# Kernel tuning notes

Hardware: AMD Instinct MI355X
Metric: run time of the kernel (lower is better)

## Reference

```python
import jax, jax.numpy as jnp
import numpy as np

B, DEC_T, ENC_T = 64, 128, 1024
H, ENC_D, ATTN, VOCAB = 512, 512, 512, 128


def setup_inputs() -> dict:
    key = jax.random.key(0)
    ks = jax.random.split(key, 12)
    s = 0.05
    return {
        "inputs": jax.random.randint(ks[0], (B, DEC_T), 0, 127),
        "encoder_outputs": jax.random.normal(ks[1], (B, ENC_T, ENC_D), jnp.float32),
        "embedding": jax.random.normal(ks[2], (VOCAB, H), jnp.float32) * s,
        "w_ih": jax.random.normal(ks[3], (3 * H, H + ENC_D), jnp.float32) * s,
        "w_hh": jax.random.normal(ks[4], (3 * H, H), jnp.float32) * s,
        "b_ih": jnp.zeros((3 * H,), jnp.float32),
        "b_hh": jnp.zeros((3 * H,), jnp.float32),
        "attn_wq": jax.random.normal(ks[5], (ATTN, H), jnp.float32) * s,
        "attn_wv": jax.random.normal(ks[6], (ATTN, ENC_D), jnp.float32) * s,
        "attn_conv_w": jax.random.normal(ks[7], (ATTN, 1, 3), jnp.float32) * s,
        "attn_conv_b": jnp.zeros((ATTN,), jnp.float32),
        "attn_bias": jnp.zeros((ATTN,), jnp.float32),
        "attn_v": jax.random.normal(ks[8], (ATTN,), jnp.float32) * s,
        "fc_w": jax.random.normal(ks[9], (VOCAB, H + ENC_D), jnp.float32) * s,
        "fc_b": jnp.zeros((VOCAB,), jnp.float32),
    }


def reference(inputs, encoder_outputs, embedding, w_ih, w_hh, b_ih, b_hh,
              attn_wq, attn_wv, attn_conv_w, attn_conv_b, attn_bias, attn_v,
              fc_w, fc_b):
    emb = embedding[inputs]  # (B, dec_T, H); no eos in inputs so filter is identity
    # precompute encoder value projection once (reused every step)
    enc_proj = jnp.einsum('bte,ae->bta', encoder_outputs, attn_wv)  # (B, enc_T, A)

    def gru_step(h, x):
        gi = x @ w_ih.T + b_ih  # (B, 3H)
        gh = h @ w_hh.T + b_hh
        r = jax.nn.sigmoid(gi[:, :H] + gh[:, :H])
        z = jax.nn.sigmoid(gi[:, H:2 * H] + gh[:, H:2 * H])
        n = jnp.tanh(gi[:, 2 * H:] + r * gh[:, 2 * H:])
        return (1.0 - z) * n + z * h

    def step(carry, x_t):
        h, context, attn_w = carry
        rnn_in = jnp.concatenate([x_t, context], axis=1)  # (B, H+enc_D)
        h = gru_step(h, rnn_in)  # output == new hidden for 1-layer GRU
        # location-aware attention: conv over previous attention weights
        conv = jax.lax.conv_general_dilated(
            attn_w[:, None, :], attn_conv_w, (1,), ((1, 1),),
            dimension_numbers=('NCH', 'OIH', 'NCH'))  # (B, A, enc_T)
        conv_feat = conv.transpose(0, 2, 1) + attn_conv_b  # (B, enc_T, A)
        q = h @ attn_wq.T  # (B, A)
        e = jnp.tanh(q[:, None, :] + enc_proj + conv_feat + attn_bias)
        score = jnp.einsum('bta,a->bt', e, attn_v)  # (B, enc_T)
        attn_w = jax.nn.softmax(score, axis=-1)
        context = jnp.einsum('bt,bte->be', attn_w, encoder_outputs)  # (B, enc_D)
        out_cat = jnp.concatenate([h, context], axis=1)  # (B, H+enc_D)
        pred = jax.nn.log_softmax(out_cat @ fc_w.T + fc_b, axis=-1)  # (B, V)
        return (h, context, attn_w), (pred, attn_w, out_cat)

    init = (jnp.zeros((B, H), emb.dtype),
            jnp.zeros((B, ENC_D), emb.dtype),
            jnp.zeros((B, ENC_T), emb.dtype))
    _, (y, aw, oc) = jax.lax.scan(step, init, emb.transpose(1, 0, 2))
    # back to batch-major: (B, dec_T, *)
    return (y.transpose(1, 0, 2), aw.transpose(1, 0, 2), oc.transpose(1, 0, 2))
```

## Files before the change

kernel.cpp:

```cpp
#include <hip/hip_runtime.h>
#include <stdint.h>

#define BB 64
#define SS 128
#define EE 1024
#define HH 512
#define DD 512
#define AA 512
#define VV 128
#define KX 1536
#define NC 2048
#define NSC 8
#define NCP 4

#define AW_OFF ((size_t)BB*SS*VV)
#define OC_OFF (AW_OFF + (size_t)BB*SS*EE)

typedef unsigned short u16;

__device__ __forceinline__ float sigmoid_f(float x){
  return __builtin_amdgcn_rcpf(1.f + __expf(-x));
}
__device__ __forceinline__ float tanh_f(float x){
  float e = __expf(2.f*x);
  return 1.f - 2.f*__builtin_amdgcn_rcpf(e + 1.f);
}
__device__ __forceinline__ u16 f2bf(float f){
  uint32_t u = __float_as_uint(f);
  return (u16)((u + 0x7fffu + ((u>>16)&1u)) >> 16);
}

__global__ void k_build(const float* __restrict__ w_ih, const float* __restrict__ w_hh,
                        const float* __restrict__ b_ih, const float* __restrict__ b_hh,
                        const float* __restrict__ wq,   const float* __restrict__ wv,
                        const float* __restrict__ fc_w,
                        float* __restrict__ Wbig, float* __restrict__ wqT,
                        float* __restrict__ wvT,  float* __restrict__ fcT,
                        float* __restrict__ bias_big){
  int i = blockIdx.x*256 + threadIdx.x;
  const int NW = KX*NC;
  if (i < NW){
    int k = i >> 11, c = i & (NC-1);
    float v;
    if (c < 1024)      v = (k < 1024) ? w_ih[c*1024 + k] : w_hh[c*512 + (k-1024)];
    else if (c < 1536) v = (k < 1024) ? w_ih[c*1024 + k] : 0.f;
    else               v = (k >= 1024) ? w_hh[(c-512)*512 + (k-1024)] : 0.f;
    Wbig[i] = v; return;
  }
  i -= NW;
  if (i < 512*512){ int j = i >> 9, a = i & 511; wqT[i] = wq[a*512 + j]; return; }
  i -= 512*512;
  if (i < 512*512){ int e = i >> 9, a = i & 511; wvT[i] = wv[a*512 + e]; return; }
  i -= 512*512;
  if (i < 1024*128){ int k = i >> 7, v = i & 127; fcT[i] = fc_w[v*1024 + k]; return; }
  i -= 1024*128;
  if (i < NC){
    float bv;
    if (i < 1024)      bv = b_ih[i] + b_hh[i];
    else if (i < 1536) bv = b_ih[i];
    else               bv = b_hh[i - 512];
    bias_big[i] = bv;
  }
}

__global__ __launch_bounds__(256) void k_encp(const float* __restrict__ enc,
                                              const float* __restrict__ wvT,
                                              const float* __restrict__ abias,
                                              const float* __restrict__ convb,
                                              u16* __restrict__ encp){
  __shared__ float As[64][36];
  __shared__ float Bs[32][68];
  int tid = threadIdx.x;
  int r0 = blockIdx.x * 64;
  int a0 = blockIdx.y * 64;
  float4 acc[4];
  #pragma unroll
  for (int r = 0; r < 4; ++r) acc[r] = make_float4(0.f,0.f,0.f,0.f);
  int rl = tid >> 2, kl0 = (tid & 3) * 8;
  int kl2 = tid >> 3, al0 = (tid & 7) * 8;
  int br = (tid >> 4) * 4, cc = (tid & 15) * 4;
  for (int kk = 0; kk < 512; kk += 32){
    float4 av0 = *(const float4*)&enc[(size_t)(r0+rl)*512 + kk + kl0];
    float4 av1 = *(const float4*)&enc[(size_t)(r0+rl)*512 + kk + kl0 + 4];
    float4 bv0 = *(const float4*)&wvT[(size_t)(kk+kl2)*512 + a0 + al0];
    float4 bv1 = *(const float4*)&wvT[(size_t)(kk+kl2)*512 + a0 + al0 + 4];
    __syncthreads();
    *(float4*)&As[rl][kl0]     = av0;
    *(float4*)&As[rl][kl0+4]   = av1;
    *(float4*)&Bs[kl2][al0]    = bv0;
    *(float4*)&Bs[kl2][al0+4]  = bv1;
    __syncthreads();
    #pragma unroll
    for (int i = 0; i < 32; ++i){
      float4 b4 = *(const float4*)&Bs[i][cc];
      float x0 = As[br][i], x1 = As[br+1][i], x2 = As[br+2][i], x3 = As[br+3][i];
      acc[0].x += x0*b4.x; acc[0].y += x0*b4.y; acc[0].z += x0*b4.z; acc[0].w += x0*b4.w;
      acc[1].x += x1*b4.x; acc[1].y += x1*b4.y; acc[1].z += x1*b4.z; acc[1].w += x1*b4.w;
      acc[2].x += x2*b4.x; acc[2].y += x2*b4.y; acc[2].z += x2*b4.z; acc[2].w += x2*b4.w;
      acc[3].x += x3*b4.x; acc[3].y += x3*b4.y; acc[3].z += x3*b4.z; acc[3].w += x3*b4.w;
    }
  }
  int a = a0 + cc;
  float b0f = abias[a]   + convb[a];
  float b1f = abias[a+1] + convb[a+1];
  float b2f_ = abias[a+2] + convb[a+2];
  float b3f = abias[a+3] + convb[a+3];
  #pragma unroll
  for (int r = 0; r < 4; ++r){
    size_t row = (size_t)(r0 + br + r);
    ushort4 pk;
    pk.x = f2bf(acc[r].x + b0f);
    pk.y = f2bf(acc[r].y + b1f);
    pk.z = f2bf(acc[r].z + b2f_);
    pk.w = f2bf(acc[r].w + b3f);
    *(ushort4*)&encp[row*512 + a] = pk;
  }
}

__global__ __launch_bounds__(256) void k_encbf(const float* __restrict__ enc,
                                               u16* __restrict__ enc_bf){
  size_t i = ((size_t)blockIdx.x*256 + threadIdx.x) * 4;
  float4 v = *(const float4*)&enc[i];
  ushort4 pk;
  pk.x = f2bf(v.x); pk.y = f2bf(v.y); pk.z = f2bf(v.z); pk.w = f2bf(v.w);
  *(ushort4*)&enc_bf[i] = pk;
}

__global__ __launch_bounds__(256) void k_ggemm_fc(const int* __restrict__ inputs,
                                                  const float* __restrict__ emb,
                                                  const float* __restrict__ ctxp,
                                                  const float* __restrict__ sump,
                                                  const float* __restrict__ h,
                                                  const float* __restrict__ Wbig,
                                                  float* __restrict__ Gp,
                                                  const float* __restrict__ fcT,
                                                  const float* __restrict__ fc_b,
                                                  float* __restrict__ rs_buf,
                                                  float* __restrict__ out,
                                                  int s, int gemm_nb, int sfc){
  int tid = threadIdx.x;
  if ((int)blockIdx.x < gemm_nb){
    __shared__ float Xs[64][36];
    __shared__ float Ws[32][68];
    __shared__ float rs_l[64];
    int bid = blockIdx.x;
    int c0 = (bid & 31) * 64;
    int kc = bid >> 5;
    int kbase = kc * 192;
    bool t0 = (s == 0);
    if (!t0 && tid < 64){
      float ssum = 0.f;
      #pragma unroll
      for (int p2 = 0; p2 < NSC; ++p2) ssum += sump[p2*64 + tid];
      rs_l[tid] = __builtin_amdgcn_rcpf(ssum);
    }
    float4 acc[4];
    #pragma unroll
    for (int r = 0; r < 4; ++r) acc[r] = make_float4(0.f,0.f,0.f,0.f);
    int bl = tid >> 2, kl0 = (tid & 3) * 8;
    int kw = tid >> 3, cl0 = (tid & 7) * 8;
    int br = (tid >> 4) * 4, cc = (tid & 15) * 4;
    const float* emb_b = emb + (size_t)inputs[bl*SS + s]*HH;
    __syncthreads();
    for (int kk = 0; kk < 192; kk += 32){
      float xv[8];
      #pragma unroll
      for (int u = 0; u < 8; ++u){
        int kg = kbase + kk + kl0 + u;
        float v;
        if (kg < 512)       v = emb_b[kg];
        else if (kg < 1024){
          if (t0) v = 0.f;
          else {
            int d = kg - 512;
            float t = 0.f;
            #pragma unroll
            for (int p2 = 0; p2 < NCP; ++p2) t += ctxp[(size_t)(p2*64+bl)*512 + d];
            v = t * rs_l[bl];
          }
        }
        else                v = t0 ? 0.f : h[bl*512 + kg - 1024];
        xv[u] = v;
      }
      float4 w1 = *(const float4*)&Wbig[(size_t)(kbase+kk+kw)*NC + c0 + cl0];
      float4 w2 = *(const float4*)&Wbig[(size_t)(kbase+kk+kw)*NC + c0 + cl0 + 4];
      __syncthreads();
      *(float4*)&Xs[bl][kl0]   = make_float4(xv[0],xv[1],xv[2],xv[3]);
      *(float4*)&Xs[bl][kl0+4] = make_float4(xv[4],xv[5],xv[6],xv[7]);
      *(float4*)&Ws[kw][cl0]   = w1;
      *(float4*)&Ws[kw][cl0+4] = w2;
      __syncthreads();
      #pragma unroll
      for (int i = 0; i < 32; ++i){
        float4 b4 = *(const float4*)&Ws[i][cc];
        float x0 = Xs[br][i], x1 = Xs[br+1][i], x2 = Xs[br+2][i], x3 = Xs[br+3][i];
        acc[0].x += x0*b4.x; acc[0].y += x0*b4.y; acc[0].z += x0*b4.z; acc[0].w += x0*b4.w;
        acc[1].x += x1*b4.x; acc[1].y += x1*b4.y; acc[1].z += x1*b4.z; acc[1].w += x1*b4.w;
        acc[2].x += x2*b4.x; acc[2].y += x2*b4.y; acc[2].z += x2*b4.z; acc[2].w += x2*b4.w;
        acc[3].x += x3*b4.x; acc[3].y += x3*b4.y; acc[3].z += x3*b4.z; acc[3].w += x3*b4.w;
      }
    }
    #pragma unroll
    for (int r = 0; r < 4; ++r)
      *(float4*)&Gp[(size_t)(kc*64 + br + r)*NC + c0 + cc] = acc[r];
  } else {
    if (sfc < 0) return;
    __shared__ float oc_l[1024];
    __shared__ float lp[2][128];
    __shared__ float l_l[128];
    int b = blockIdx.x - gemm_nb;
    float ssum = 0.f;
    #pragma unroll
    for (int p2 = 0; p2 < NSC; ++p2) ssum += sump[p2*64 + b];
    float rs = __builtin_amdgcn_rcpf(ssum);
    if (tid == 0) rs_buf[b] = rs;
    oc_l[tid]       = h[b*512 + tid];
    oc_l[tid + 256] = h[b*512 + tid + 256];
    int d0 = tid*2;
    float a0 = 0.f, a1 = 0.f;
    #pragma unroll
    for (int cc2 = 0; cc2 < NCP; ++cc2){
      float2 p2v = *(const float2*)&ctxp[(size_t)(cc2*64 + b)*512 + d0];
      a0 += p2v.x; a1 += p2v.y;
    }
    a0 *= rs; a1 *= rs;
    oc_l[512 + d0]     = a0;
    oc_l[512 + d0 + 1] = a1;
    size_t oco = OC_OFF + (size_t)(b*SS + sfc)*1024 + 512 + d0;
    out[oco]     = a0;
    out[oco + 1] = a1;
    __syncthreads();
    int v = tid & 127, half = tid >> 7;
    float acc = 0.f;
    #pragma unroll 8
    for (int k = 0; k < 512; ++k)
      acc += oc_l[half*512 + k] * fcT[(size_t)(half*512 + k)*128 + v];
    lp[half][v] = acc;
    __syncthreads();
    if (tid < 128) l_l[tid] = lp[0][tid] + lp[1][tid] + fc_b[tid];
    __syncthreads();
    if (tid < 128){
      float m = -1e30f;
      for (int i = 0; i < 128; ++i) m = fmaxf(m, l_l[i]);
      float sm = 0.f;
      for (int i = 0; i < 128; ++i) sm += __expf(l_l[i] - m);
      out[(size_t)(b*SS + sfc)*VV + tid] = l_l[tid] - m - __logf(sm);
    }
  }
}

__global__ __launch_bounds__(256) void k_gate_q(const float* __restrict__ Gp,
                                                const float* __restrict__ bias_big,
                                                float* __restrict__ h,
                                                const float* __restrict__ wqT,
                                                float* __restrict__ qp,
                                                float* __restrict__ out, int s){
  __shared__ float h_l[512];
  int tid = threadIdx.x;
  int jt = blockIdx.x, bt = blockIdx.y;
  bool t0 = (s == 0);
  #pragma unroll
  for (int it = 0; it < 2; ++it){
    int item = tid + it*256;
    int bi = item >> 6, jl = item & 63;
    int b = bt*8 + bi, j = jt*64 + jl;
    float s0=0.f, s1=0.f, s2=0.f, s3=0.f;
    #pragma unroll
    for (int kc = 0; kc < 8; ++kc){
      const float* g = Gp + (size_t)(kc*64 + b)*NC;
      s0 += g[j]; s1 += g[512+j]; s2 += g[1024+j]; s3 += g[1536+j];
    }
    float r = sigmoid_f(s0 + bias_big[j]);
    float z = sigmoid_f(s1 + bias_big[512+j]);
    float n = tanh_f(s2 + bias_big[1024+j] + r*(s3 + bias_big[1536+j]));
    float hold = t0 ? 0.f : h[b*512 + j];
    float hn = (1.f - z)*n + z*hold;
    h_l[item] = hn;
    h[b*512 + j] = hn;
    out[OC_OFF + (size_t)(b*SS + s)*1024 + j] = hn;
  }
  __syncthreads();
  int a0 = tid*2;
  float2 acc8[8];
  #pragma unroll
  for (int bi = 0; bi < 8; ++bi) acc8[bi] = make_float2(0.f, 0.f);
  for (int j = 0; j < 64; ++j){
    float2 w = *(const float2*)&wqT[(size_t)(jt*64 + j)*512 + a0];
    #pragma unroll
    for (int bi = 0; bi < 8; ++bi){
      float hv = h_l[bi*64 + j];
      acc8[bi].x += hv*w.x; acc8[bi].y += hv*w.y;
    }
  }
  #pragma unroll
  for (int bi = 0; bi < 8; ++bi)
    *(float2*)&qp[(size_t)(jt*64 + bt*8 + bi)*512 + a0] = acc8[bi];
}

__global__ __launch_bounds__(1024, 8) void k_score(const float* __restrict__ qp,
                                                   const float* __restrict__ attn_v,
                                                   const float* __restrict__ conv_w,
                                                   const u16* __restrict__ encp,
                                                   const float* __restrict__ expsc_prev,
                                                   float* __restrict__ expsc_cur,
                                                   const float* __restrict__ rs_buf,
                                                   float* __restrict__ sump,
                                                   float* __restrict__ out, int s){
  __shared__ float q_l[512], v_l[512], c0_l[512], c1_l[512], c2_l[512];
  __shared__ float ew_l[128];
  int tid = threadIdx.x;
  int et = blockIdx.x, b = blockIdx.y;
  if (tid < 512){
    float qq = 0.f;
    #pragma unroll
    for (int jt = 0; jt < 8; ++jt) qq += qp[(size_t)(jt*64 + b)*512 + tid];
    q_l[tid]  = qq;
    v_l[tid]  = attn_v[tid];
    c0_l[tid] = conv_w[tid*3 + 0];
    c1_l[tid] = conv_w[tid*3 + 1];
    c2_l[tid] = conv_w[tid*3 + 2];
  }
  __syncthreads();
  int wave = tid >> 6, lane = tid & 63;
  float q8[8], v8[8], c08[8], c18[8], c28[8];
  #pragma unroll
  for (int i = 0; i < 8; ++i){
    int a = lane*8 + i;
    q8[i] = q_l[a]; v8[i] = v_l[a]; c08[i] = c0_l[a]; c18[i] = c1_l[a]; c28[i] = c2_l[a];
  }
  float rs_prev = (s > 0) ? rs_buf[b] : 0.f;
  const float* prev = expsc_prev + (size_t)b*EE;
  #pragma unroll
  for (int eu = 0; eu < 8; ++eu){
    int e_loc = wave*8 + eu;
    int e = et*128 + e_loc;
    float wl = 0.f, wc = 0.f, wr = 0.f;
    if (s > 0){
      wc = prev[e] * rs_prev;
      wl = (e > 0)    ? prev[e-1]*rs_prev : 0.f;
      wr = (e < EE-1) ? prev[e+1]*rs_prev : 0.f;
    }
    uint4 pk = *(const uint4*)(encp + ((size_t)(b*EE + e)*512 + lane*8));
    uint32_t ua[4] = {pk.x, pk.y, pk.z, pk.w};
    float acc = 0.f;
    #pragma unroll
    for (int p = 0; p < 4; ++p){
      float plo = __uint_as_float(ua[p] << 16);
      float phi = __uint_as_float(ua[p] & 0xffff0000u);
      int ii = p*2;
      float v0 = q8[ii]   + plo + c08[ii]*wl   + c18[ii]*wc   + c28[ii]*wr;
      acc += tanh_f(v0) * v8[ii];
      float v1 = q8[ii+1] + phi + c08[ii+1]*wl + c18[ii+1]*wc + c28[ii+1]*wr;
      acc += tanh_f(v1) * v8[ii+1];
    }
    #pragma unroll
    for (int off = 32; off; off >>= 1) acc += __shfl_xor(acc, off, 64);
    if (lane == 0) ew_l[e_loc] = __expf(acc);
  }
  __syncthreads();
  if (tid < 128){
    int e = et*128 + tid;
    expsc_cur[(size_t)b*EE + e] = ew_l[tid];
    if (s > 0) out[AW_OFF + (size_t)(b*SS + (s-1))*EE + e] = prev[e]*rs_prev;
  }
  if (tid < 64){
    float t2 = ew_l[tid] + ew_l[tid + 64];
    #pragma unroll
    for (int off = 32; off; off >>= 1) t2 += __shfl_xor(t2, off, 64);
    if (tid == 0) sump[et*64 + b] = t2;
  }
}

__global__ __launch_bounds__(512, 8) void k_ctx(const u16* __restrict__ enc_bf,
                                                const float* __restrict__ expsc_cur,
                                                float* __restrict__ ctxp){
  __shared__ float w_l[256];
  __shared__ float redc[8][512];
  int tid = threadIdx.x;
  int c = blockIdx.x, b = blockIdx.y;
  if (tid < 256) w_l[tid] = expsc_cur[(size_t)b*EE + c*256 + tid];
  __syncthreads();
  int es = tid >> 6, lane = tid & 63;
  int d0 = lane * 8;
  float acc8[8];
  #pragma unroll
  for (int i = 0; i < 8; ++i) acc8[i] = 0.f;
  #pragma unroll 4
  for (int i = 0; i < 32; ++i){
    int e_loc = es*32 + i;
    uint4 pk = *(const uint4*)(enc_bf + ((size_t)(b*EE + c*256 + e_loc)*512 + d0));
    float w = w_l[e_loc];
    uint32_t ua[4] = {pk.x, pk.y, pk.z, pk.w};
    #pragma unroll
    for (int p = 0; p < 4; ++p){
      acc8[p*2]   += w * __uint_as_float(ua[p] << 16);
      acc8[p*2+1] += w * __uint_as_float(ua[p] & 0xffff0000u);
    }
  }
  #pragma unroll
  for (int i = 0; i < 8; ++i) redc[es][d0 + i] = acc8[i];
  __syncthreads();
  if (tid < 128){
    int d = tid * 4;
    float4 t = make_float4(0.f,0.f,0.f,0.f);
    #pragma unroll
    for (int e2 = 0; e2 < 8; ++e2){
      float4 r4 = *(const float4*)&redc[e2][d];
      t.x += r4.x; t.y += r4.y; t.z += r4.z; t.w += r4.w;
    }
    *(float4*)&ctxp[(size_t)(c*64 + b)*512 + d] = t;
  }
}

__global__ __launch_bounds__(256) void k_tail(const float* __restrict__ h,
                                              const float* __restrict__ ctxp,
                                              const float* __restrict__ sump,
                                              const float* __restrict__ expsc,
                                              const float* __restrict__ fcT,
                                              const float* __restrict__ fc_b,
                                              float* __restrict__ out){
  __shared__ float oc_l[1024];
  __shared__ float lp[2][128];
  __shared__ float l_l[128];
  int tid = threadIdx.x, b = blockIdx.x;
  const int sfc = SS - 1;
  float ssum = 0.f;
  #pragma unroll
  for (int p2 = 0; p2 < NSC; ++p2) ssum += sump[p2*64 + b];
  float rs = __builtin_amdgcn_rcpf(ssum);
  #pragma unroll
  for (int i = 0; i < 4; ++i){
    int e = i*256 + tid;
    out[AW_OFF + (size_t)(b*SS + sfc)*EE + e] = expsc[(size_t)b*EE + e] * rs;
  }
  oc_l[tid]       = h[b*512 + tid];
  oc_l[tid + 256] = h[b*512 + tid + 256];
  int d0 = tid*2;
  float a0 = 0.f, a1 = 0.f;
  #pragma unroll
  for (int cc2 = 0; cc2 < NCP; ++cc2){
    float2 p2v = *(const float2*)&ctxp[(size_t)(cc2*64 + b)*512 + d0];
    a0 += p2v.x; a1 += p2v.y;
  }
  a0 *= rs; a1 *= rs;
  oc_l[512 + d0]     = a0;
  oc_l[512 + d0 + 1] = a1;
  size_t oco = OC_OFF + (size_t)(b*SS + sfc)*1024 + 512 + d0;
  out[oco]     = a0;
  out[oco + 1] = a1;
  __syncthreads();
  int v = tid & 127, half = tid >> 7;
  float acc = 0.f;
  #pragma unroll 8
  for (int k = 0; k < 512; ++k)
    acc += oc_l[half*512 + k] * fcT[(size_t)(half*512 + k)*128 + v];
  lp[half][v] = acc;
  __syncthreads();
  if (tid < 128) l_l[tid] = lp[0][tid] + lp[1][tid] + fc_b[tid];
  __syncthreads();
  if (tid < 128){
    float m = -1e30f;
    for (int i = 0; i < 128; ++i) m = fmaxf(m, l_l[i]);
    float sm = 0.f;
    for (int i = 0; i < 128; ++i) sm += __expf(l_l[i] - m);
    out[(size_t)(b*SS + sfc)*VV + tid] = l_l[tid] - m - __logf(sm);
  }
}

extern "C" void kernel_launch(void* const* d_in, const int* in_sizes, int n_in,
                              void* d_out, int out_size, void* d_ws, size_t ws_size,
                              hipStream_t stream){
  (void)in_sizes; (void)n_in; (void)out_size; (void)ws_size;
  const int*   inputs = (const int*)d_in[0];
  const float* enc    = (const float*)d_in[1];
  const float* emb    = (const float*)d_in[2];
  const float* w_ih   = (const float*)d_in[3];
  const float* w_hh   = (const float*)d_in[4];
  const float* b_ih   = (const float*)d_in[5];
  const float* b_hh   = (const float*)d_in[6];
  const float* wq     = (const float*)d_in[7];
  const float* wv     = (const float*)d_in[8];
  const float* convw  = (const float*)d_in[9];
  const float* convb  = (const float*)d_in[10];
  const float* abias  = (const float*)d_in[11];
  const float* av     = (const float*)d_in[12];
  const float* fcw    = (const float*)d_in[13];
  const float* fcb    = (const float*)d_in[14];
  float* out = (float*)d_out;

  char* p = (char*)d_ws;
  auto alloc = [&](size_t bytes)->char*{
    char* r = p; p += (bytes + 255) & ~(size_t)255; return r;
  };
  u16*   encp   = (u16*)  alloc((size_t)BB*EE*AA*2);
  u16*   enc_bf = (u16*)  alloc((size_t)BB*EE*DD*2);
  float* Wbig   = (float*)alloc((size_t)KX*NC*4);
  float* wqT    = (float*)alloc((size_t)512*512*4);
  float* wvT    = (float*)alloc((size_t)512*512*4);
  float* fcT    = (float*)alloc((size_t)1024*128*4);
  float* biasb  = (float*)alloc((size_t)NC*4);
  float* hbuf   = (float*)alloc((size_t)BB*HH*4);
  float* Gp     = (float*)alloc((size_t)8*BB*NC*4);
  float* qp     = (float*)alloc((size_t)8*BB*AA*4);
  float* exps0  = (float*)alloc((size_t)BB*EE*4);
  float* exps1  = (float*)alloc((size_t)BB*EE*4);
  float* sump   = (float*)alloc((size_t)NSC*BB*4);
  float* ctxp   = (float*)alloc((size_t)NCP*BB*DD*4);
  float* rs_buf = (float*)alloc((size_t)BB*4);

  int total0 = KX*NC + 512*512 + 512*512 + 1024*128 + NC;
  k_build<<<(total0 + 255)/256, 256, 0, stream>>>(w_ih, w_hh, b_ih, b_hh, wq, wv, fcw,
                                                  Wbig, wqT, wvT, fcT, biasb);
  k_encp<<<dim3(1024, 8), 256, 0, stream>>>(enc, wvT, abias, convb, encp);
  k_encbf<<<(BB*EE*DD/4 + 255)/256, 256, 0, stream>>>(enc, enc_bf);

  for (int s = 0; s < SS; ++s){
    int sfc = s - 1;
    int grid = (sfc >= 0) ? 320 : 256;
    float* e_prev = (s & 1) ? exps0 : exps1;
    float* e_cur  = (s & 1) ? exps1 : exps0;
    k_ggemm_fc<<<grid, 256, 0, stream>>>(inputs, emb, ctxp, sump, hbuf, Wbig, Gp,
                                         fcT, fcb, rs_buf, out, s, 256, sfc);
    k_gate_q<<<dim3(8, 8), 256, 0, stream>>>(Gp, biasb, hbuf, wqT, qp, out, s);
    k_score<<<dim3(8, 64), 1024, 0, stream>>>(qp, av, convw, encp,
                                              e_prev, e_cur, rs_buf, sump, out, s);
    k_ctx<<<dim3(4, 64), 512, 0, stream>>>(enc_bf, e_cur, ctxp);
  }
  k_tail<<<64, 256, 0, stream>>>(hbuf, ctxp, sump, exps1, fcT, fcb, out);
}
```

Measured before the change: 10.62 ms.

## Replace per-step kernel launches with persistent kernel using grid barriers

```diff
diff --git a/kernel.cpp b/kernel.cpp
--- a/kernel.cpp
+++ b/kernel.cpp
@@ -10,8 +10,10 @@
 #define VV 128
 #define KX 1536
 #define NC 2048
-#define NSC 8
+#define NKC 6
+#define NSC 4
 #define NCP 4
+#define NBLK 256
 
 #define AW_OFF ((size_t)BB*SS*VV)
 #define OC_OFF (AW_OFF + (size_t)BB*SS*EE)
@@ -126,344 +128,357 @@
   *(ushort4*)&enc_bf[i] = pk;
 }
 
-__global__ __launch_bounds__(256) void k_ggemm_fc(const int* __restrict__ inputs,
-                                                  const float* __restrict__ emb,
-                                                  const float* __restrict__ ctxp,
-                                                  const float* __restrict__ sump,
-                                                  const float* __restrict__ h,
-                                                  const float* __restrict__ Wbig,
-                                                  float* __restrict__ Gp,
-                                                  const float* __restrict__ fcT,
-                                                  const float* __restrict__ fc_b,
-                                                  float* __restrict__ rs_buf,
-                                                  float* __restrict__ out,
-                                                  int s, int gemm_nb, int sfc){
-  int tid = threadIdx.x;
-  if ((int)blockIdx.x < gemm_nb){
-    __shared__ float Xs[64][36];
-    __shared__ float Ws[32][68];
-    __shared__ float rs_l[64];
-    int bid = blockIdx.x;
-    int c0 = (bid & 31) * 64;
-    int kc = bid >> 5;
-    int kbase = kc * 192;
-    bool t0 = (s == 0);
-    if (!t0 && tid < 64){
+__device__ __forceinline__ void gbar(unsigned* bar, int bid){
+  __syncthreads();
+  if (threadIdx.x == 0){
+    unsigned* cnt1 = bar + (bid >> 4) * 32;
+    unsigned* cnt2 = bar + 512;
+    unsigned* gen  = bar + 544;
+    unsigned g = __hip_atomic_load(gen, __ATOMIC_RELAXED, __HIP_MEMORY_SCOPE_AGENT);
+    unsigned o1 = __hip_atomic_fetch_add(cnt1, 1u, __ATOMIC_ACQ_REL, __HIP_MEMORY_SCOPE_AGENT);
+    if (o1 == 15u){
+      __hip_atomic_store(cnt1, 0u, __ATOMIC_RELAXED, __HIP_MEMORY_SCOPE_AGENT);
+      unsigned o2 = __hip_atomic_fetch_add(cnt2, 1u, __ATOMIC_ACQ_REL, __HIP_MEMORY_SCOPE_AGENT);
+      if (o2 == 15u){
+        __hip_atomic_store(cnt2, 0u, __ATOMIC_RELAXED, __HIP_MEMORY_SCOPE_AGENT);
+        __hip_atomic_store(gen, g + 1u, __ATOMIC_RELEASE, __HIP_MEMORY_SCOPE_AGENT);
+      } else {
+        while (__hip_atomic_load(gen, __ATOMIC_ACQUIRE, __HIP_MEMORY_SCOPE_AGENT) == g)
+          __builtin_amdgcn_s_sleep(2);
+      }
+    } else {
+      while (__hip_atomic_load(gen, __ATOMIC_ACQUIRE, __HIP_MEMORY_SCOPE_AGENT) == g)
+        __builtin_amdgcn_s_sleep(2);
+    }
+  }
+  __syncthreads();
+}
+
+struct SmA { float Xs[64][36]; float Ws[32][68]; float rs_l[64]; };
+struct SmF { float oc[1024]; float lp[2][128]; float ll[128]; };
+struct SmB { float h_l[512]; };
+struct SmC { float q[512]; float v[512]; float c0[512]; float c1[512];
+             float c2[512]; float pw[260]; float ew[256]; float redc[8][512]; };
+union Smem { SmA a; SmF f; SmB b; SmC c; };
+
+__device__ __forceinline__ float score8(uint4 pk, float wl, float wc, float wr,
+                                        const float* q8, const float* v8,
+                                        const float* c08, const float* c18,
+                                        const float* c28){
+  uint32_t ua[4] = {pk.x, pk.y, pk.z, pk.w};
+  float acc = 0.f;
+  #pragma unroll
+  for (int p = 0; p < 4; ++p){
+    float plo = __uint_as_float(ua[p] << 16);
+    float phi = __uint_as_float(ua[p] & 0xffff0000u);
+    int ii = p*2;
+    float x0 = q8[ii]   + plo + c08[ii]*wl   + c18[ii]*wc   + c28[ii]*wr;
+    acc += tanh_f(x0) * v8[ii];
+    float x1 = q8[ii+1] + phi + c08[ii+1]*wl + c18[ii+1]*wc + c28[ii+1]*wr;
+    acc += tanh_f(x1) * v8[ii+1];
+  }
+  return acc;
+}
+
+__global__ __launch_bounds__(512, 2) void k_persist(
+    const int* __restrict__ inputs, const float* __restrict__ emb,
+    const float* __restrict__ Wbig, const float* __restrict__ biasb,
+    const float* __restrict__ wqT,  const float* __restrict__ fcT,
+    const float* __restrict__ fcb,  const float* __restrict__ av,
+    const float* __restrict__ convw,
+    const u16* __restrict__ encp,   const u16* __restrict__ enc_bf,
+    float* __restrict__ Gp, float* __restrict__ qp, float* __restrict__ hbuf,
+    float* __restrict__ exps0, float* __restrict__ exps1,
+    float* __restrict__ sump, float* __restrict__ ctxp,
+    float* __restrict__ rs_buf, unsigned* bar, float* __restrict__ out)
+{
+  __shared__ Smem sm;
+  const int tid = threadIdx.x, bid = blockIdx.x;
+
+  for (int s = 0; s < SS; ++s){
+    const bool t0 = (s == 0);
+    const float* eprev = (s & 1) ? exps0 : exps1;
+    float*       ecur  = (s & 1) ? exps1 : exps0;
+
+    if (bid < 192){
+      const int c0 = (bid & 31) * 64;
+      const int kc = bid >> 5;
+      const int kbase = kc * 256;
+      if (!t0 && tid < 64){
+        float ssum = 0.f;
+        #pragma unroll
+        for (int p2 = 0; p2 < NSC; ++p2) ssum += sump[p2*64 + tid];
+        sm.a.rs_l[tid] = __builtin_amdgcn_rcpf(ssum);
+      }
+      const int bl = tid >> 3, kl0 = (tid & 7) * 4;
+      const int kw = tid >> 4, cl0 = (tid & 15) * 4;
+      const int br = (tid >> 4) * 2, cc = (tid & 15) * 4;
+      const float* emb_b = emb + (size_t)inputs[bl*SS + s]*HH;
+      float4 acc0 = make_float4(0.f,0.f,0.f,0.f);
+      float4 acc1 = make_float4(0.f,0.f,0.f,0.f);
+      __syncthreads();
+      for (int kk = 0; kk < 256; kk += 32){
+        float xv[4];
+        #pragma unroll
+        for (int u = 0; u < 4; ++u){
+          int kg = kbase + kk + kl0 + u;
+          float v;
+          if (kg < 512)       v = emb_b[kg];
+          else if (kg < 1024){
+            if (t0) v = 0.f;
+            else {
+              int d = kg - 512;
+              float t = 0.f;
+              #pragma unroll
+              for (int p2 = 0; p2 < NCP; ++p2) t += ctxp[(size_t)(p2*64+bl)*512 + d];
+              v = t * sm.a.rs_l[bl];
+            }
+          }
+          else                v = t0 ? 0.f : hbuf[bl*512 + kg - 1024];
+          xv[u] = v;
+        }
+        float4 w1 = *(const float4*)&Wbig[(size_t)(kbase+kk+kw)*NC + c0 + cl0];
+        __syncthreads();
+        *(float4*)&sm.a.Xs[bl][kl0] = make_float4(xv[0],xv[1],xv[2],xv[3]);
+        *(float4*)&sm.a.Ws[kw][cl0] = w1;
+        __syncthreads();
+        #pragma unroll
+        for (int i = 0; i < 32; ++i){
+          float4 b4 = *(const float4*)&sm.a.Ws[i][cc];
+          float x0 = sm.a.Xs[br][i], x1 = sm.a.Xs[br+1][i];
+          acc0.x += x0*b4.x; acc0.y += x0*b4.y; acc0.z += x0*b4.z; acc0.w += x0*b4.w;
+          acc1.x += x1*b4.x; acc1.y += x1*b4.y; acc1.z += x1*b4.z; acc1.w += x1*b4.w;
+        }
+      }
+      *(float4*)&Gp[(size_t)(kc*64 + br    )*NC + c0 + cc] = acc0;
+      *(float4*)&Gp[(size_t)(kc*64 + br + 1)*NC + c0 + cc] = acc1;
+    } else if (!t0){
+      const int b = bid - 192;
       float ssum = 0.f;
       #pragma unroll
-      for (int p2 = 0; p2 < NSC; ++p2) ssum += sump[p2*64 + tid];
-      rs_l[tid] = __builtin_amdgcn_rcpf(ssum);
-    }
-    float4 acc[4];
-    #pragma unroll
-    for (int r = 0; r < 4; ++r) acc[r] = make_float4(0.f,0.f,0.f,0.f);
-    int bl = tid >> 2, kl0 = (tid & 3) * 8;
-    int kw = tid >> 3, cl0 = (tid & 7) * 8;
-    int br = (tid >> 4) * 4, cc = (tid & 15) * 4;
-    const float* emb_b = emb + (size_t)inputs[bl*SS + s]*HH;
-    __syncthreads();
-    for (int kk = 0; kk < 192; kk += 32){
-      float xv[8];
-      #pragma unroll
-      for (int u = 0; u < 8; ++u){
-        int kg = kbase + kk + kl0 + u;
-        float v;
-        if (kg < 512)       v = emb_b[kg];
-        else if (kg < 1024){
-          if (t0) v = 0.f;
-          else {
-            int d = kg - 512;
-            float t = 0.f;
-            #pragma unroll
-            for (int p2 = 0; p2 < NCP; ++p2) t += ctxp[(size_t)(p2*64+bl)*512 + d];
-            v = t * rs_l[bl];
-          }
-        }
-        else                v = t0 ? 0.f : h[bl*512 + kg - 1024];
-        xv[u] = v;
-      }
-      float4 w1 = *(const float4*)&Wbig[(size_t)(kbase+kk+kw)*NC + c0 + cl0];
-      float4 w2 = *(const float4*)&Wbig[(size_t)(kbase+kk+kw)*NC + c0 + cl0 + 4];
-      __syncthreads();
-      *(float4*)&Xs[bl][kl0]   = make_float4(xv[0],xv[1],xv[2],xv[3]);
-      *(float4*)&Xs[bl][kl0+4] = make_float4(xv[4],xv[5],xv[6],xv[7]);
-      *(float4*)&Ws[kw][cl0]   = w1;
-      *(float4*)&Ws[kw][cl0+4] = w2;
-      __syncthreads();
-      #pragma unroll
+      for (int p2 = 0; p2 < NSC; ++p2) ssum += sump[p2*64 + b];
+      const float rs = __builtin_amdgcn_rcpf(ssum);
+      if (tid == 0) rs_buf[b] = rs;
+      if (tid < 256){
+        sm.f.oc[tid]     = hbuf[b*512 + tid];
+        sm.f.oc[tid+256] = hbuf[b*512 + tid + 256];
+        int d0 = tid*2;
+        float a0 = 0.f, a1 = 0.f;
+        #pragma unroll
+        for (int cc2 = 0; cc2 < NCP; ++cc2){
+          float2 pv = *(const float2*)&ctxp[(size_t)(cc2*64 + b)*512 + d0];
+          a0 += pv.x; a1 += pv.y;
+        }
+        a0 *= rs; a1 *= rs;
+        sm.f.oc[512+d0]   = a0;
+        sm.f.oc[512+d0+1] = a1;
+        size_t oco = OC_OFF + (size_t)(b*SS + (s-1))*1024 + 512 + d0;
+        out[oco]     = a0;
+        out[oco + 1] = a1;
+      }
+      __syncthreads();
+      if (tid < 256){
+        int v = tid & 127, half = tid >> 7;
+        float acc = 0.f;
+        #pragma unroll 8
+        for (int k = 0; k < 512; ++k)
+          acc += sm.f.oc[half*512 + k] * fcT[(size_t)(half*512 + k)*128 + v];
+        sm.f.lp[half][v] = acc;
+      }
+      __syncthreads();
+      if (tid < 128) sm.f.ll[tid] = sm.f.lp[0][tid] + sm.f.lp[1][tid] + fcb[tid];
+      __syncthreads();
+      if (tid < 128){
+        float m = -1e30f;
+        for (int i = 0; i < 128; ++i) m = fmaxf(m, sm.f.ll[i]);
+        float smm = 0.f;
+        for (int i = 0; i < 128; ++i) smm += __expf(sm.f.ll[i] - m);
+        out[(size_t)(b*SS + (s-1))*VV + tid] = sm.f.ll[tid] - m - __logf(smm);
+      }
+    }
+    gbar(bar, bid);
+
+    if (bid < 64){
+      const int jt = bid & 7, bt = bid >> 3;
+      const int bi = tid >> 6, jl = tid & 63;
+      const int b = bt*8 + bi, j = jt*64 + jl;
+      float s0=0.f, s1=0.f, s2=0.f, s3=0.f;
+      #pragma unroll
+      for (int kc = 0; kc < NKC; ++kc){
+        const float* g = Gp + (size_t)(kc*64 + b)*NC;
+        s0 += g[j]; s1 += g[512+j]; s2 += g[1024+j]; s3 += g[1536+j];
+      }
+      float r = sigmoid_f(s0 + biasb[j]);
+      float z = sigmoid_f(s1 + biasb[512+j]);
+      float n = tanh_f(s2 + biasb[1024+j] + r*(s3 + biasb[1536+j]));
+      float hold = t0 ? 0.f : hbuf[b*512 + j];
+      float hn = (1.f - z)*n + z*hold;
+      sm.b.h_l[tid] = hn;
+      hbuf[b*512 + j] = hn;
+      out[OC_OFF + (size_t)(b*SS + s)*1024 + j] = hn;
+      __syncthreads();
+      const int a = tid;
+      float acc8[8];
+      #pragma unroll
+      for (int q2 = 0; q2 < 8; ++q2) acc8[q2] = 0.f;
+      for (int jj = 0; jj < 64; ++jj){
+        float w = wqT[(size_t)(jt*64 + jj)*512 + a];
+        #pragma unroll
+        for (int b2 = 0; b2 < 8; ++b2) acc8[b2] += sm.b.h_l[b2*64 + jj]*w;
+      }
+      #pragma unroll
+      for (int b2 = 0; b2 < 8; ++b2)
+        qp[(size_t)(jt*64 + bt*8 + b2)*512 + a] = acc8[b2];
+    }
+    gbar(bar, bid);
+
+    {
+      const int b = bid & 63, et = bid >> 6;
+      const float rs_prev = t0 ? 0.f : rs_buf[b];
+      const float* prev = eprev + (size_t)b*EE;
+      {
+        float qq = 0.f;
+        #pragma unroll
+        for (int jt2 = 0; jt2 < 8; ++jt2) qq += qp[(size_t)(jt2*64 + b)*512 + tid];
+        sm.c.q[tid]  = qq;
+        sm.c.v[tid]  = av[tid];
+        sm.c.c0[tid] = convw[tid*3 + 0];
+        sm.c.c1[tid] = convw[tid*3 + 1];
+        sm.c.c2[tid] = convw[tid*3 + 2];
+        if (tid < 258){
+          int e = et*256 - 1 + tid;
+          float w = 0.f;
+          if (!t0 && e >= 0 && e < EE) w = prev[e] * rs_prev;
+          sm.c.pw[tid] = w;
+        }
+      }
+      __syncthreads();
+      if (!t0 && tid < 256)
+        out[AW_OFF + (size_t)(b*SS + (s-1))*EE + et*256 + tid] = sm.c.pw[tid+1];
+      const int wave = tid >> 6, lane = tid & 63;
+      float q8[8], v8[8], c08[8], c18[8], c28[8];
+      #pragma unroll
+      for (int i = 0; i < 8; ++i){
+        int a = lane*8 + i;
+        q8[i] = sm.c.q[a]; v8[i] = sm.c.v[a];
+        c08[i] = sm.c.c0[a]; c18[i] = sm.c.c1[a]; c28[i] = sm.c.c2[a];
+      }
+      const size_t enc_base = ((size_t)b*EE + et*256)*512 + lane*8;
+      #pragma unroll 2
+      for (int i0 = 0; i0 < 32; i0 += 4){
+        const int el = wave*32 + i0;
+        uint4 pk0 = *(const uint4*)(encp + enc_base + (size_t)(el  )*512);
+        uint4 pk1 = *(const uint4*)(encp + enc_base + (size_t)(el+1)*512);
+        uint4 pk2 = *(const uint4*)(encp + enc_base + (size_t)(el+2)*512);
+        uint4 pk3 = *(const uint4*)(encp + enc_base + (size_t)(el+3)*512);
+        float a0 = score8(pk0, sm.c.pw[el],   sm.c.pw[el+1], sm.c.pw[el+2], q8,v8,c08,c18,c28);
+        float a1 = score8(pk1, sm.c.pw[el+1], sm.c.pw[el+2], sm.c.pw[el+3], q8,v8,c08,c18,c28);
+        float a2 = score8(pk2, sm.c.pw[el+2], sm.c.pw[el+3], sm.c.pw[el+4], q8,v8,c08,c18,c28);
+        float a3 = score8(pk3, sm.c.pw[el+3], sm.c.pw[el+4], sm.c.pw[el+5], q8,v8,c08,c18,c28);
+        #pragma unroll
+        for (int off = 32; off; off >>= 1){
+          a0 += __shfl_xor(a0, off, 64);
+          a1 += __shfl_xor(a1, off, 64);
+          a2 += __shfl_xor(a2, off, 64);
+          a3 += __shfl_xor(a3, off, 64);
+        }
+        if (lane == 0){
+          sm.c.ew[el]   = __expf(a0);
+          sm.c.ew[el+1] = __expf(a1);
+          sm.c.ew[el+2] = __expf(a2);
+          sm.c.ew[el+3] = __expf(a3);
+        }
+      }
+      __syncthreads();
+      if (tid < 256) ecur[(size_t)b*EE + et*256 + tid] = sm.c.ew[tid];
+      if (tid < 64){
+        float t2 = sm.c.ew[tid] + sm.c.ew[tid+64] + sm.c.ew[tid+128] + sm.c.ew[tid+192];
+        #pragma unroll
+        for (int off = 32; off; off >>= 1) t2 += __shfl_xor(t2, off, 64);
+        if (tid == 0) sump[et*64 + b] = t2;
+      }
+      const int d0 = lane * 8;
+      float acc8[8];
+      #pragma unroll
+      for (int i = 0; i < 8; ++i) acc8[i] = 0.f;
+      const size_t encb_base = ((size_t)b*EE + et*256)*512 + d0;
+      #pragma unroll 4
       for (int i = 0; i < 32; ++i){
-        float4 b4 = *(const float4*)&Ws[i][cc];
-        float x0 = Xs[br][i], x1 = Xs[br+1][i], x2 = Xs[br+2][i], x3 = Xs[br+3][i];
-        acc[0].x += x0*b4.x; acc[0].y += x0*b4.y; acc[0].z += x0*b4.z; acc[0].w += x0*b4.w;
-        acc[1].x += x1*b4.x; acc[1].y += x1*b4.y; acc[1].z += x1*b4.z; acc[1].w += x1*b4.w;
-        acc[2].x += x2*b4.x; acc[2].y += x2*b4.y; acc[2].z += x2*b4.z; acc[2].w += x2*b4.w;
-        acc[3].x += x3*b4.x; acc[3].y += x3*b4.y; acc[3].z += x3*b4.z; acc[3].w += x3*b4.w;
-      }
-    }
-    #pragma unroll
-    for (int r = 0; r < 4; ++r)
-      *(float4*)&Gp[(size_t)(kc*64 + br + r)*NC + c0 + cc] = acc[r];
-  } else {
-    if (sfc < 0) return;
-    __shared__ float oc_l[1024];
-    __shared__ float lp[2][128];
-    __shared__ float l_l[128];
-    int b = blockIdx.x - gemm_nb;
+        int el2 = wave*32 + i;
+        uint4 pk = *(const uint4*)(enc_bf + encb_base + (size_t)el2*512);
+        float w = sm.c.ew[el2];
+        uint32_t ua[4] = {pk.x, pk.y, pk.z, pk.w};
+        #pragma unroll
+        for (int p = 0; p < 4; ++p){
+          acc8[p*2]   += w * __uint_as_float(ua[p] << 16);
+          acc8[p*2+1] += w * __uint_as_float(ua[p] & 0xffff0000u);
+        }
+      }
+      #pragma unroll
+      for (int i = 0; i < 8; ++i) sm.c.redc[wave][d0 + i] = acc8[i];
+      __syncthreads();
+      if (tid < 128){
+        int d = tid * 4;
+        float4 t = make_float4(0.f,0.f,0.f,0.f);
+        #pragma unroll
+        for (int w2 = 0; w2 < 8; ++w2){
+          float4 r4 = *(const float4*)&sm.c.redc[w2][d];
+          t.x += r4.x; t.y += r4.y; t.z += r4.z; t.w += r4.w;
+        }
+        *(float4*)&ctxp[(size_t)(et*64 + b)*512 + d] = t;
+      }
+    }
+    gbar(bar, bid);
+  }
+
+  if (bid < 64){
+    const int b = bid;
+    const float* efin = exps1;
     float ssum = 0.f;
     #pragma unroll
     for (int p2 = 0; p2 < NSC; ++p2) ssum += sump[p2*64 + b];
-    float rs = __builtin_amdgcn_rcpf(ssum);
-    if (tid == 0) rs_buf[b] = rs;
-    oc_l[tid]       = h[b*512 + tid];
-    oc_l[tid + 256] = h[b*512 + tid + 256];
-    int d0 = tid*2;
-    float a0 = 0.f, a1 = 0.f;
-    #pragma unroll
-    for (int cc2 = 0; cc2 < NCP; ++cc2){
-      float2 p2v = *(const float2*)&ctxp[(size_t)(cc2*64 + b)*512 + d0];
-      a0 += p2v.x; a1 += p2v.y;
-    }
-    a0 *= rs; a1 *= rs;
-    oc_l[512 + d0]     = a0;
-    oc_l[512 + d0 + 1] = a1;
-    size_t oco = OC_OFF + (size_t)(b*SS + sfc)*1024 + 512 + d0;
-    out[oco]     = a0;
-    out[oco + 1] = a1;
+    const float rs = __builtin_amdgcn_rcpf(ssum);
+    if (tid < 256){
+      #pragma unroll
+      for (int i = 0; i < 4; ++i){
+        int e = i*256 + tid;
+        out[AW_OFF + (size_t)(b*SS + (SS-1))*EE + e] = efin[(size_t)b*EE + e] * rs;
+      }
+      sm.f.oc[tid]     = hbuf[b*512 + tid];
+      sm.f.oc[tid+256] = hbuf[b*512 + tid + 256];
+      int d0 = tid*2;
+      float a0 = 0.f, a1 = 0.f;
+      #pragma unroll
+      for (int cc2 = 0; cc2 < NCP; ++cc2){
+        float2 pv = *(const float2*)&ctxp[(size_t)(cc2*64 + b)*512 + d0];
+        a0 += pv.x; a1 += pv.y;
+      }
+      a0 *= rs; a1 *= rs;
+      sm.f.oc[512+d0]   = a0;
+      sm.f.oc[512+d0+1] = a1;
+      size_t oco = OC_OFF + (size_t)(b*SS + (SS-1))*1024 + 512 + d0;
+      out[oco]     = a0;
+      out[oco + 1] = a1;
+    }
     __syncthreads();
-    int v = tid & 127, half = tid >> 7;
-    float acc = 0.f;
-    #pragma unroll 8
-    for (int k = 0; k < 512; ++k)
-      acc += oc_l[half*512 + k] * fcT[(size_t)(half*512 + k)*128 + v];
-    lp[half][v] = acc;
+    if (tid < 256){
+      int v = tid & 127, half = tid >> 7;
+      float acc = 0.f;
+      #pragma unroll 8
+      for (int k = 0; k < 512; ++k)
+        acc += sm.f.oc[half*512 + k] * fcT[(size_t)(half*512 + k)*128 + v];
+      sm.f.lp[half][v] = acc;
+    }
     __syncthreads();
-    if (tid < 128) l_l[tid] = lp[0][tid] + lp[1][tid] + fc_b[tid];
+    if (tid < 128) sm.f.ll[tid] = sm.f.lp[0][tid] + sm.f.lp[1][tid] + fcb[tid];
     __syncthreads();
     if (tid < 128){
       float m = -1e30f;
-      for (int i = 0; i < 128; ++i) m = fmaxf(m, l_l[i]);
-      float sm = 0.f;
-      for (int i = 0; i < 128; ++i) sm += __expf(l_l[i] - m);
-      out[(size_t)(b*SS + sfc)*VV + tid] = l_l[tid] - m - __logf(sm);
-    }
-  }
-}
-
-__global__ __launch_bounds__(256) void k_gate_q(const float* __restrict__ Gp,
-                                                const float* __restrict__ bias_big,
-                                                float* __restrict__ h,
-                                                const float* __restrict__ wqT,
-                                                float* __restrict__ qp,
-                                                float* __restrict__ out, int s){
-  __shared__ float h_l[512];
-  int tid = threadIdx.x;
-  int jt = blockIdx.x, bt = blockIdx.y;
-  bool t0 = (s == 0);
-  #pragma unroll
-  for (int it = 0; it < 2; ++it){
-    int item = tid + it*256;
-    int bi = item >> 6, jl = item & 63;
-    int b = bt*8 + bi, j = jt*64 + jl;
-    float s0=0.f, s1=0.f, s2=0.f, s3=0.f;
-    #pragma unroll
-    for (int kc = 0; kc < 8; ++kc){
-      const float* g = Gp + (size_t)(kc*64 + b)*NC;
-      s0 += g[j]; s1 += g[512+j]; s2 += g[1024+j]; s3 += g[1536+j];
-    }
-    float r = sigmoid_f(s0 + bias_big[j]);
-    float z = sigmoid_f(s1 + bias_big[512+j]);
-    float n = tanh_f(s2 + bias_big[1024+j] + r*(s3 + bias_big[1536+j]));
-    float hold = t0 ? 0.f : h[b*512 + j];
-    float hn = (1.f - z)*n + z*hold;
-    h_l[item] = hn;
-    h[b*512 + j] = hn;
-    out[OC_OFF + (size_t)(b*SS + s)*1024 + j] = hn;
-  }
-  __syncthreads();
-  int a0 = tid*2;
-  float2 acc8[8];
-  #pragma unroll
-  for (int bi = 0; bi < 8; ++bi) acc8[bi] = make_float2(0.f, 0.f);
-  for (int j = 0; j < 64; ++j){
-    float2 w = *(const float2*)&wqT[(size_t)(jt*64 + j)*512 + a0];
-    #pragma unroll
-    for (int bi = 0; bi < 8; ++bi){
-      float hv = h_l[bi*64 + j];
-      acc8[bi].x += hv*w.x; acc8[bi].y += hv*w.y;
-    }
-  }
-  #pragma unroll
-  for (int bi = 0; bi < 8; ++bi)
-    *(float2*)&qp[(size_t)(jt*64 + bt*8 + bi)*512 + a0] = acc8[bi];
-}
-
-__global__ __launch_bounds__(1024, 8) void k_score(const float* __restrict__ qp,
-                                                   const float* __restrict__ attn_v,
-                                                   const float* __restrict__ conv_w,
-                                                   const u16* __restrict__ encp,
-                                                   const float* __restrict__ expsc_prev,
-                                                   float* __restrict__ expsc_cur,
-                                                   const float* __restrict__ rs_buf,
-                                                   float* __restrict__ sump,
-                                                   float* __restrict__ out, int s){
-  __shared__ float q_l[512], v_l[512], c0_l[512], c1_l[512], c2_l[512];
-  __shared__ float ew_l[128];
-  int tid = threadIdx.x;
-  int et = blockIdx.x, b = blockIdx.y;
-  if (tid < 512){
-    float qq = 0.f;
-    #pragma unroll
-    for (int jt = 0; jt < 8; ++jt) qq += qp[(size_t)(jt*64 + b)*512 + tid];
-    q_l[tid]  = qq;
-    v_l[tid]  = attn_v[tid];
-    c0_l[tid] = conv_w[tid*3 + 0];
-    c1_l[tid] = conv_w[tid*3 + 1];
-    c2_l[tid] = conv_w[tid*3 + 2];
-  }
-  __syncthreads();
-  int wave = tid >> 6, lane = tid & 63;
-  float q8[8], v8[8], c08[8], c18[8], c28[8];
-  #pragma unroll
-  for (int i = 0; i < 8; ++i){
-    int a = lane*8 + i;
-    q8[i] = q_l[a]; v8[i] = v_l[a]; c08[i] = c0_l[a]; c18[i] = c1_l[a]; c28[i] = c2_l[a];
-  }
-  float rs_prev = (s > 0) ? rs_buf[b] : 0.f;
-  const float* prev = expsc_prev + (size_t)b*EE;
-  #pragma unroll
-  for (int eu = 0; eu < 8; ++eu){
-    int e_loc = wave*8 + eu;
-    int e = et*128 + e_loc;
-    float wl = 0.f, wc = 0.f, wr = 0.f;
-    if (s > 0){
-      wc = prev[e] * rs_prev;
-      wl = (e > 0)    ? prev[e-1]*rs_prev : 0.f;
-      wr = (e < EE-1) ? prev[e+1]*rs_prev : 0.f;
-    }
-    uint4 pk = *(const uint4*)(encp + ((size_t)(b*EE + e)*512 + lane*8));
-    uint32_t ua[4] = {pk.x, pk.y, pk.z, pk.w};
-    float acc = 0.f;
-    #pragma unroll
-    for (int p = 0; p < 4; ++p){
-      float plo = __uint_as_float(ua[p] << 16);
-      float phi = __uint_as_float(ua[p] & 0xffff0000u);
-      int ii = p*2;
-      float v0 = q8[ii]   + plo + c08[ii]*wl   + c18[ii]*wc   + c28[ii]*wr;
-      acc += tanh_f(v0) * v8[ii];
-      float v1 = q8[ii+1] + phi + c08[ii+1]*wl + c18[ii+1]*wc + c28[ii+1]*wr;
-      acc += tanh_f(v1) * v8[ii+1];
-    }
-    #pragma unroll
-    for (int off = 32; off; off >>= 1) acc += __shfl_xor(acc, off, 64);
-    if (lane == 0) ew_l[e_loc] = __expf(acc);
-  }
-  __syncthreads();
-  if (tid < 128){
-    int e = et*128 + tid;
-    expsc_cur[(size_t)b*EE + e] = ew_l[tid];
-    if (s > 0) out[AW_OFF + (size_t)(b*SS + (s-1))*EE + e] = prev[e]*rs_prev;
-  }
-  if (tid < 64){
-    float t2 = ew_l[tid] + ew_l[tid + 64];
-    #pragma unroll
-    for (int off = 32; off; off >>= 1) t2 += __shfl_xor(t2, off, 64);
-    if (tid == 0) sump[et*64 + b] = t2;
-  }
-}
-
-__global__ __launch_bounds__(512, 8) void k_ctx(const u16* __restrict__ enc_bf,
-                                                const float* __restrict__ expsc_cur,
-                                                float* __restrict__ ctxp){
-  __shared__ float w_l[256];
-  __shared__ float redc[8][512];
-  int tid = threadIdx.x;
-  int c = blockIdx.x, b = blockIdx.y;
-  if (tid < 256) w_l[tid] = expsc_cur[(size_t)b*EE + c*256 + tid];
-  __syncthreads();
-  int es = tid >> 6, lane = tid & 63;
-  int d0 = lane * 8;
-  float acc8[8];
-  #pragma unroll
-  for (int i = 0; i < 8; ++i) acc8[i] = 0.f;
-  #pragma unroll 4
-  for (int i = 0; i < 32; ++i){
-    int e_loc = es*32 + i;
-    uint4 pk = *(const uint4*)(enc_bf + ((size_t)(b*EE + c*256 + e_loc)*512 + d0));
-    float w = w_l[e_loc];
-    uint32_t ua[4] = {pk.x, pk.y, pk.z, pk.w};
-    #pragma unroll
-    for (int p = 0; p < 4; ++p){
-      acc8[p*2]   += w * __uint_as_float(ua[p] << 16);
-      acc8[p*2+1] += w * __uint_as_float(ua[p] & 0xffff0000u);
-    }
-  }
-  #pragma unroll
-  for (int i = 0; i < 8; ++i) redc[es][d0 + i] = acc8[i];
-  __syncthreads();
-  if (tid < 128){
-    int d = tid * 4;
-    float4 t = make_float4(0.f,0.f,0.f,0.f);
-    #pragma unroll
-    for (int e2 = 0; e2 < 8; ++e2){
-      float4 r4 = *(const float4*)&redc[e2][d];
-      t.x += r4.x; t.y += r4.y; t.z += r4.z; t.w += r4.w;
-    }
-    *(float4*)&ctxp[(size_t)(c*64 + b)*512 + d] = t;
-  }
-}
-
-__global__ __launch_bounds__(256) void k_tail(const float* __restrict__ h,
-                                              const float* __restrict__ ctxp,
-                                              const float* __restrict__ sump,
-                                              const float* __restrict__ expsc,
-                                              const float* __restrict__ fcT,
-                                              const float* __restrict__ fc_b,
-                                              float* __restrict__ out){
-  __shared__ float oc_l[1024];
-  __shared__ float lp[2][128];
-  __shared__ float l_l[128];
-  int tid = threadIdx.x, b = blockIdx.x;
-  const int sfc = SS - 1;
-  float ssum = 0.f;
-  #pragma unroll
-  for (int p2 = 0; p2 < NSC; ++p2) ssum += sump[p2*64 + b];
-  float rs = __builtin_amdgcn_rcpf(ssum);
-  #pragma unroll
-  for (int i = 0; i < 4; ++i){
-    int e = i*256 + tid;
-    out[AW_OFF + (size_t)(b*SS + sfc)*EE + e] = expsc[(size_t)b*EE + e] * rs;
-  }
-  oc_l[tid]       = h[b*512 + tid];
-  oc_l[tid + 256] = h[b*512 + tid + 256];
-  int d0 = tid*2;
-  float a0 = 0.f, a1 = 0.f;
-  #pragma unroll
-  for (int cc2 = 0; cc2 < NCP; ++cc2){
-    float2 p2v = *(const float2*)&ctxp[(size_t)(cc2*64 + b)*512 + d0];
-    a0 += p2v.x; a1 += p2v.y;
-  }
-  a0 *= rs; a1 *= rs;
-  oc_l[512 + d0]     = a0;
-  oc_l[512 + d0 + 1] = a1;
-  size_t oco = OC_OFF + (size_t)(b*SS + sfc)*1024 + 512 + d0;
-  out[oco]     = a0;
-  out[oco + 1] = a1;
-  __syncthreads();
-  int v = tid & 127, half = tid >> 7;
-  float acc = 0.f;
-  #pragma unroll 8
-  for (int k = 0; k < 512; ++k)
-    acc += oc_l[half*512 + k] * fcT[(size_t)(half*512 + k)*128 + v];
-  lp[half][v] = acc;
-  __syncthreads();
-  if (tid < 128) l_l[tid] = lp[0][tid] + lp[1][tid] + fc_b[tid];
-  __syncthreads();
-  if (tid < 128){
-    float m = -1e30f;
-    for (int i = 0; i < 128; ++i) m = fmaxf(m, l_l[i]);
-    float sm = 0.f;
-    for (int i = 0; i < 128; ++i) sm += __expf(l_l[i] - m);
-    out[(size_t)(b*SS + sfc)*VV + tid] = l_l[tid] - m - __logf(sm);
+      for (int i = 0; i < 128; ++i) m = fmaxf(m, sm.f.ll[i]);
+      float smm = 0.f;
+      for (int i = 0; i < 128; ++i) smm += __expf(sm.f.ll[i] - m);
+      out[(size_t)(b*SS + (SS-1))*VV + tid] = sm.f.ll[tid] - m - __logf(smm);
+    }
   }
 }
 
@@ -500,31 +515,24 @@
   float* fcT    = (float*)alloc((size_t)1024*128*4);
   float* biasb  = (float*)alloc((size_t)NC*4);
   float* hbuf   = (float*)alloc((size_t)BB*HH*4);
-  float* Gp     = (float*)alloc((size_t)8*BB*NC*4);
+  float* Gp     = (float*)alloc((size_t)NKC*BB*NC*4);
   float* qp     = (float*)alloc((size_t)8*BB*AA*4);
   float* exps0  = (float*)alloc((size_t)BB*EE*4);
   float* exps1  = (float*)alloc((size_t)BB*EE*4);
   float* sump   = (float*)alloc((size_t)NSC*BB*4);
   float* ctxp   = (float*)alloc((size_t)NCP*BB*DD*4);
   float* rs_buf = (float*)alloc((size_t)BB*4);
-
+  unsigned* bar = (unsigned*)alloc(4096);
+
+  hipMemsetAsync(bar, 0, 4096, stream);
   int total0 = KX*NC + 512*512 + 512*512 + 1024*128 + NC;
   k_build<<<(total0 + 255)/256, 256, 0, stream>>>(w_ih, w_hh, b_ih, b_hh, wq, wv, fcw,
                                                   Wbig, wqT, wvT, fcT, biasb);
   k_encp<<<dim3(1024, 8), 256, 0, stream>>>(enc, wvT, abias, convb, encp);
   k_encbf<<<(BB*EE*DD/4 + 255)/256, 256, 0, stream>>>(enc, enc_bf);
 
-  for (int s = 0; s < SS; ++s){
-    int sfc = s - 1;
-    int grid = (sfc >= 0) ? 320 : 256;
-    float* e_prev = (s & 1) ? exps0 : exps1;
-    float* e_cur  = (s & 1) ? exps1 : exps0;
-    k_ggemm_fc<<<grid, 256, 0, stream>>>(inputs, emb, ctxp, sump, hbuf, Wbig, Gp,
-                                         fcT, fcb, rs_buf, out, s, 256, sfc);
-    k_gate_q<<<dim3(8, 8), 256, 0, stream>>>(Gp, biasb, hbuf, wqT, qp, out, s);
-    k_score<<<dim3(8, 64), 1024, 0, stream>>>(qp, av, convw, encp,
-                                              e_prev, e_cur, rs_buf, sump, out, s);
-    k_ctx<<<dim3(4, 64), 512, 0, stream>>>(enc_bf, e_cur, ctxp);
-  }
-  k_tail<<<64, 256, 0, stream>>>(hbuf, ctxp, sump, exps1, fcT, fcb, out);
-}
+  k_persist<<<NBLK, 512, 0, stream>>>(inputs, emb, Wbig, biasb, wqT, fcT, fcb,
+                                      av, convw, encp, enc_bf,
+                                      Gp, qp, hbuf, exps0, exps1,
+                                      sump, ctxp, rs_buf, bar, out);
+}
```

After: 22.83 ms. 115% more time.
